# Kernel tuning notes

Hardware: AMD Instinct MI355X
Metric: run time of the kernel (lower is better)

The kernel has to match this reference:

```python
import jax, jax.numpy as jnp
import numpy as np

B, S, D, H = 2, 2048, 1024, 16
DH = D // H  # per-head dim = 64


def setup_inputs() -> dict:
    key = jax.random.key(0)
    k0, k1, k2, k3, k4, k5 = jax.random.split(key, 6)
    x = jax.random.normal(k0, (B, S, D), dtype=jnp.float32)
    # mask: True where token is valid, False where padded ([B, S, 1] bool)
    mask = jax.random.randint(k1, (B, S, 1), 0, 2).astype(bool)
    scale = 0.02
    # Per-head projection weights stacked over heads: [H, D, DH]
    Wq = jax.random.normal(k2, (H, D, DH), dtype=jnp.float32) * scale
    Wk = jax.random.normal(k3, (H, D, DH), dtype=jnp.float32) * scale
    Wv = jax.random.normal(k4, (H, D, DH), dtype=jnp.float32) * scale
    # Output projection, torch Linear convention [out, in]: y = out @ Wo.T
    Wo = jax.random.normal(k5, (D, D), dtype=jnp.float32) * scale
    return {"x": x, "mask": mask, "Wq": Wq, "Wk": Wk, "Wv": Wv, "Wo": Wo}


def reference(x, mask, Wq, Wk, Wv, Wo):
    # Batched per-head projections (equivalent to the per-head Linear loop)
    q = jnp.einsum('bsd,hde->bhse', x, Wq)  # [B,H,S,DH]
    k = jnp.einsum('bsd,hde->bhse', x, Wk)
    v = jnp.einsum('bsd,hde->bhse', x, Wv)
    scale = 1.0 / np.sqrt(DH).astype(np.float32)
    scores = jnp.einsum('bhqe,bhke->bhqk', q, k) * scale  # [B,H,S,S]
    key_mask = mask[:, None, None, :, 0]   # [B,1,1,S]
    qry_mask = mask[:, None, :, :]          # [B,1,S,1]
    # masked keys get -1e10 added (same as original: +(~key_mask)*-1e10)
    scores = scores + (~key_mask) * jnp.float32(-1e10)
    attn = jax.nn.softmax(scores, axis=-1)
    attn = attn * qry_mask                  # zero rows for padded queries
    ctx = jnp.einsum('bhqk,bhke->bhqe', attn, v)  # [B,H,S,DH]
    # concat heads along last dim (head h -> contiguous slice, matches torch.cat)
    out = ctx.transpose(0, 2, 1, 3).reshape(B, S, D)
    return out @ Wo.T
```

## Files before the change

### kernel.cpp

```cpp
#include <hip/hip_runtime.h>
#include <hip/hip_bf16.h>

typedef __attribute__((ext_vector_type(8))) short sh8;
typedef __attribute__((ext_vector_type(4))) float f32x4;

#define LDC 136
#define QSCALE 0.18033688f
#define KMBF16 0xF14Au

#define EXP2F(x) __builtin_amdgcn_exp2f(x)

__device__ __forceinline__ void glds16(const unsigned short* g, unsigned short* l){
  __builtin_amdgcn_global_load_lds(
      (const __attribute__((address_space(1))) unsigned int*)g,
      (__attribute__((address_space(3))) unsigned int*)l, 16, 0, 0);
}

__device__ __forceinline__ unsigned short f2bf(float f){
  union { float f; unsigned u; } c; c.f = f;
  unsigned u = c.u;
  u += 0x7fffu + ((u >> 16) & 1u);
  return (unsigned short)(u >> 16);
}

__device__ __forceinline__ unsigned long long pack4bf(float a, float b, float c, float d){
  __hip_bfloat162 lo = __float22bfloat162_rn(make_float2(a, b));
  __hip_bfloat162 hi = __float22bfloat162_rn(make_float2(c, d));
  union { unsigned u[2]; unsigned long long ull; } pk;
  pk.u[0] = *(unsigned*)&lo; pk.u[1] = *(unsigned*)&hi;
  return pk.ull;
}

__global__ __launch_bounds__(256) void cvt_bf16_2(const float* __restrict__ s0,
                                                  unsigned short* __restrict__ d0, int n0,
                                                  const float* __restrict__ s1,
                                                  unsigned short* __restrict__ d1, int n1){
  int i = blockIdx.x*256 + threadIdx.x;
  const float* s; unsigned short* d;
  if (i < n0){ s = s0; d = d0; }
  else if (i < n0 + n1){ s = s1; d = d1; i -= n0; }
  else return;
  float4 v = ((const float4*)s)[i];
  ushort4 o;
  o.x = f2bf(v.x); o.y = f2bf(v.y); o.z = f2bf(v.z); o.w = f2bf(v.w);
  ((ushort4*)d)[i] = o;
}

__global__ __launch_bounds__(256) void transpose_w(const float* __restrict__ Wq,
                                                   const float* __restrict__ Wk,
                                                   const float* __restrict__ Wv,
                                                   unsigned short* __restrict__ wt){
  __shared__ float tile[64][65];
  int idx = blockIdx.x;
  int jm = idx >> 8;
  int rest = idx & 255;
  int h = rest >> 4, dt = rest & 15;
  const float* src = (jm==0 ? Wq : (jm==1 ? Wk : Wv)) + (size_t)h*65536;
  int t = threadIdx.x;
  {
    int r = t >> 2, c0 = (t & 3)*16;
    for (int i=0;i<4;++i){
      float4 v = *(const float4*)&src[(size_t)(dt*64 + r)*64 + c0 + i*4];
      tile[r][c0+i*4+0]=v.x; tile[r][c0+i*4+1]=v.y; tile[r][c0+i*4+2]=v.z; tile[r][c0+i*4+3]=v.w;
    }
  }
  __syncthreads();
  {
    int e = t >> 2, r0 = (t & 3)*16;
    int j = jm*1024 + h*64 + e;
    __align__(16) unsigned short buf[16];
    for (int i=0;i<16;++i) buf[i] = f2bf(tile[r0+i][e]);
    *(uint4*)&wt[(size_t)j*1024 + dt*64 + r0    ] = *(uint4*)&buf[0];
    *(uint4*)&wt[(size_t)j*1024 + dt*64 + r0 + 8] = *(uint4*)&buf[8];
  }
}

template<int BM>
__global__ __launch_bounds__(256) void gemm_bt(const unsigned short* __restrict__ A,
                                               const unsigned short* __restrict__ Bt,
                                               unsigned short* __restrict__ Cq,
                                               unsigned short* __restrict__ Ck,
                                               unsigned short* __restrict__ Cv,
                                               float* __restrict__ Cf,
                                               int M, int N, int K, int mode){
  constexpr int MI = BM/32;
  constexpr int ABUF = BM*64;
  constexpr int DBUFN = 2*ABUF + 2*8192;
  constexpr int SMEMN = (DBUFN > 17408) ? DBUFN : 17408;
  __shared__ __align__(16) unsigned short smem[SMEMN];
  const int t = threadIdx.x;
  const int w = t >> 6, lane = t & 63, l15 = lane & 15, quad = lane >> 4;

  int lin = blockIdx.y * gridDim.x + blockIdx.x;
  int gn = gridDim.x;
  int per = 8 * gn;
  int gid = lin / per, rem = lin % per;
  int j = rem / gn, nc = rem % gn;
  const int m0 = (gid*8 + j) * BM;
  const int n0 = nc * 128;

  const int wm = (w >> 1)*(BM/2), wn = (w & 1)*64;
  const int lr8 = lane >> 3;
  const int gc8 = (lane & 7) ^ lr8;
  const int h7 = l15 & 7;
  f32x4 acc[MI][4] = {};

  auto stage = [&](int k0, int bb){
    unsigned short* as = smem + bb*ABUF;
    unsigned short* bs = smem + 2*ABUF + bb*8192;
    for (int p = 0; p < BM/32; ++p){
      int rbase = p*32 + w*8;
      glds16(&A [(size_t)(m0 + rbase + lr8)*K + k0 + gc8*8], &as[rbase*64]);
    }
    for (int p = 0; p < 4; ++p){
      int rbase = p*32 + w*8;
      glds16(&Bt[(size_t)(n0 + rbase + lr8)*K + k0 + gc8*8], &bs[rbase*64]);
    }
  };

  const int NS = K >> 6;
  stage(0, 0);
  for (int ks = 0; ks < NS; ++ks){
    const int bb = ks & 1;
    __syncthreads();
    if (ks + 1 < NS) stage((ks+1)*64, bb ^ 1);
    const unsigned short* as = smem + bb*ABUF;
    const unsigned short* bs = smem + 2*ABUF + bb*8192;
    for (int kk = 0; kk < 2; ++kk){
      const int cs = (((kk<<2) + quad) ^ h7) * 8;
      sh8 aF[MI], bF[4];
      for (int i = 0; i < MI; ++i)
        aF[i] = *(const sh8*)&as[(wm + i*16 + l15)*64 + cs];
      for (int i = 0; i < 4; ++i)
        bF[i] = *(const sh8*)&bs[(wn + i*16 + l15)*64 + cs];
      for (int mi = 0; mi < MI; ++mi)
        for (int ni = 0; ni < 4; ++ni)
          acc[mi][ni] = __builtin_amdgcn_mfma_f32_16x16x32_bf16(aF[mi], bF[ni], acc[mi][ni], 0, 0, 0);
    }
  }

  if (mode == 2){
    for (int mi = 0; mi < MI; ++mi){
      int rowb = m0 + wm + mi*16 + quad*4;
      for (int ni = 0; ni < 4; ++ni){
        int col = n0 + wn + ni*16 + l15;
        for (int r = 0; r < 4; ++r)
          Cf[(size_t)(rowb + r)*N + col] = acc[mi][ni][r];
      }
    }
    return;
  }

  if constexpr (BM == 128){
    __syncthreads();
    unsigned short* Ct = smem;
    const bool isv = (n0 >= 2048);
    const float cscale = (n0 < 1024) ? QSCALE : 1.0f;
    for (int mi = 0; mi < 4; ++mi){
      for (int ni = 0; ni < 4; ++ni){
        for (int r = 0; r < 4; ++r){
          int lr = wm + mi*16 + quad*4 + r;
          int lc = wn + ni*16 + l15;
          unsigned short bv = f2bf(acc[mi][ni][r] * cscale);
          if (isv) Ct[lc*LDC + lr] = bv;
          else     Ct[lr*LDC + lc] = bv;
        }
      }
    }
    __syncthreads();

    const int b = m0 >> 11, sbase = m0 & 2047;
    const int hbase = (n0 & 1023) >> 6;
    if (!isv){
      unsigned short* dst = (n0 < 1024) ? Cq : Ck;
      for (int i = 0; i < 8; ++i){
        int s  = i*16 + (t >> 4);
        int hh = (t >> 3) & 1;
        int c  = t & 7;
        uint4 val = *(const uint4*)&Ct[s*LDC + hh*64 + c*8];
        int h = hbase + hh;
        *(uint4*)&dst[((size_t)(b*16 + h)*2048 + sbase + s)*64 + c*8] = val;
      }
    } else {
      for (int i = 0; i < 8; ++i){
        int ecol = i*16 + (t >> 4);
        int s0   = (t & 15)*8;
        uint4 val = *(const uint4*)&Ct[ecol*LDC + s0];
        int hh = ecol >> 6, e = ecol & 63;
        int h = hbase + hh;
        *(uint4*)&Cv[((size_t)(b*16 + h)*64 + e)*2048 + sbase + s0] = val;
      }
    }
  }
}

__global__ __launch_bounds__(512) void flash_attn(const unsigned short* __restrict__ q,
                                                  const unsigned short* __restrict__ k,
                                                  const unsigned short* __restrict__ vt,
                                                  const int* __restrict__ mask,
                                                  unsigned short* __restrict__ ctx){
  __shared__ __align__(16) unsigned short Ks[2][4096];
  __shared__ __align__(16) unsigned short Vs[2][4096];
  __shared__ __align__(16) unsigned short Ps[8][1024];
  __shared__ __align__(16) unsigned short kmb[2048];

  const int idx = blockIdx.x;
  const int xcd = idx & 7, sub = idx >> 3;
  const int bh = xcd*4 + (sub & 3);
  const int qt = sub >> 2;
  const int b = bh >> 4, h = bh & 15;
  const int t = threadIdx.x;
  const int w = t >> 6, lane = t & 63, l15 = lane & 15, quad = lane >> 4;
  const size_t base = (size_t)bh * 2048 * 64;

  const unsigned short* qp0 = q + base + (size_t)(qt*128 + w*16 + l15)*64;
  sh8 qf[2];
  qf[0] = *(const sh8*)(qp0 +      quad*8);
  qf[1] = *(const sh8*)(qp0 + 32 + quad*8);

  {
    int4 m0 = ((const int4*)(mask + b*2048))[t];
    __align__(8) unsigned short tmp[4];
    tmp[0] = m0.x ? 0 : KMBF16; tmp[1] = m0.y ? 0 : KMBF16;
    tmp[2] = m0.z ? 0 : KMBF16; tmp[3] = m0.w ? 0 : KMBF16;
    *(unsigned long long*)&kmb[t*4] = *(unsigned long long*)tmp;
  }

  const int lr8 = lane >> 3;
  const int gc8 = (lane & 7) ^ lr8;
  const int h7 = l15 & 7;
  const int cs0 = ((quad    ) ^ h7) * 8;
  const int cs1 = ((quad + 4) ^ h7) * 8;
  const int pw_off = (quad & 1)*4;
  const int pr0 = ((0*4 + quad) ^ h7) * 8;
  const int pr1 = ((1*4 + quad) ^ h7) * 8;

  auto stageKV = [&](int kt, int bb){
    int r0 = w*8;
    glds16(&k [base + (size_t)(kt*64 + r0 + lr8)*64 + gc8*8], &Ks[bb][r0*64]);
    glds16(&vt[base + (size_t)(r0 + lr8)*2048 + kt*64 + gc8*8], &Vs[bb][r0*64]);
  };

  float la[4] = {};
  f32x4 O[4] = {};

  stageKV(0, 0);
  for (int kt = 0; kt < 32; ++kt){
    const int bb = kt & 1;
    __syncthreads();
    if (kt + 1 < 32) stageKV(kt + 1, bb ^ 1);

    for (int mt = 0; mt < 4; ++mt){
      sh8 a0 = *(const sh8*)&Ks[bb][(mt*16 + l15)*64 + cs0];
      sh8 a1 = *(const sh8*)&Ks[bb][(mt*16 + l15)*64 + cs1];
      unsigned long long kq = *(const unsigned long long*)&kmb[kt*64 + mt*16 + quad*4];
      unsigned d0 = (unsigned)kq, d1 = (unsigned)(kq >> 32);
      f32x4 a;
      a[0] = __uint_as_float(d0 << 16);
      a[1] = __uint_as_float(d0 & 0xFFFF0000u);
      a[2] = __uint_as_float(d1 << 16);
      a[3] = __uint_as_float(d1 & 0xFFFF0000u);
      const int pwc = (((mt*2 + (quad>>1)) ^ h7) * 8) + pw_off;
      a = __builtin_amdgcn_mfma_f32_16x16x32_bf16(a0, qf[0], a, 0, 0, 0);
      a = __builtin_amdgcn_mfma_f32_16x16x32_bf16(a1, qf[1], a, 0, 0, 0);
      float e0 = EXP2F(a[0]); la[0] += e0;
      float e1 = EXP2F(a[1]); la[1] += e1;
      float e2 = EXP2F(a[2]); la[2] += e2;
      float e3 = EXP2F(a[3]); la[3] += e3;
      *(unsigned long long*)&Ps[w][l15*64 + pwc] = pack4bf(e0, e1, e2, e3);
    }

    sh8 pf0 = *(const sh8*)&Ps[w][l15*64 + pr0];
    sh8 pf1 = *(const sh8*)&Ps[w][l15*64 + pr1];
    for (int et = 0; et < 4; ++et){
      sh8 vf0 = *(const sh8*)&Vs[bb][(et*16 + l15)*64 + cs0];
      O[et] = __builtin_amdgcn_mfma_f32_16x16x32_bf16(vf0, pf0, O[et], 0, 0, 0);
    }
    for (int et = 0; et < 4; ++et){
      sh8 vf1 = *(const sh8*)&Vs[bb][(et*16 + l15)*64 + cs1];
      O[et] = __builtin_amdgcn_mfma_f32_16x16x32_bf16(vf1, pf1, O[et], 0, 0, 0);
    }
  }

  {
    float l_i = (la[0] + la[1]) + (la[2] + la[3]);
    l_i += __shfl_xor(l_i, 16);
    l_i += __shfl_xor(l_i, 32);
    int srow = qt*128 + w*16 + l15;
    bool qm = (kmb[srow] == 0);
    float inv = (qm && l_i > 0.f) ? 1.f/l_i : 0.f;
    unsigned short* crow = ctx + (((size_t)b*2048 + srow)*16 + h)*64;
    for (int et = 0; et < 4; ++et)
      *(unsigned long long*)&crow[et*16 + quad*4] =
        pack4bf(O[et][0]*inv, O[et][1]*inv, O[et][2]*inv, O[et][3]*inv);
  }
}

extern "C" void kernel_launch(void* const* d_in, const int* in_sizes, int n_in,
                              void* d_out, int out_size, void* d_ws, size_t ws_size,
                              hipStream_t stream){
  const float* x  = (const float*)d_in[0];
  const int* mask = (const int*)  d_in[1];
  const float* Wq = (const float*)d_in[2];
  const float* Wk = (const float*)d_in[3];
  const float* Wv = (const float*)d_in[4];
  const float* Wo = (const float*)d_in[5];
  float* out = (float*)d_out;

  char* ws = (char*)d_ws;
  unsigned short* x_bf  = (unsigned short*)(ws);
  unsigned short* wt    = (unsigned short*)(ws + 8388608);
  unsigned short* wo_bf = (unsigned short*)(ws + 14680064);
  unsigned short* qb    = (unsigned short*)(ws + 16777216);
  unsigned short* kb    = (unsigned short*)(ws + 25165824);
  unsigned short* vtb   = (unsigned short*)(ws + 33554432);
  unsigned short* ctx   = (unsigned short*)(ws + 41943040);

  cvt_bf16_2<<<5120, 256, 0, stream>>>(x, x_bf, 1048576, Wo, wo_bf, 262144);
  transpose_w<<<768, 256, 0, stream>>>(Wq, Wk, Wv, wt);
  gemm_bt<128><<<dim3(24, 32), 256, 0, stream>>>(x_bf, wt, qb, kb, vtb, nullptr, 4096, 3072, 1024, 0);
  flash_attn<<<512, 512, 0, stream>>>(qb, kb, vtb, mask, ctx);
  gemm_bt<64><<<dim3(8, 64), 256, 0, stream>>>(ctx, wo_bf, nullptr, nullptr, nullptr, out, 4096, 1024, 1024, 2);
}
```

Baseline: 184.4 us.

## Split attention over key halves and pass P through registers via permlane swaps

Attention now splits the key sequence in two, launching twice as many blocks. Each block writes unnormalized partial outputs and row sums, and a new reduce kernel adds the halves, normalizes and applies the query mask. Separately, the P tile no longer goes through a shared-memory round trip: the bf16 probabilities are rearranged with v_permlane32/16_swap to form the MFMA B operand directly, which frees LDS and removes per-tile LDS traffic. The trade-off is an extra launch and an extra read/write of two bf16 partial buffers, plus bf16 rounding of the partials before summation.

```diff
diff --git a/kernel.cpp b/kernel.cpp
--- a/kernel.cpp
+++ b/kernel.cpp
@@ -29,6 +29,13 @@
   union { unsigned u[2]; unsigned long long ull; } pk;
   pk.u[0] = *(unsigned*)&lo; pk.u[1] = *(unsigned*)&hi;
   return pk.ull;
+}
+
+__device__ __forceinline__ void pl32swap(unsigned &a, unsigned &b){
+  asm volatile("v_permlane32_swap_b32 %0, %1" : "+v"(a), "+v"(b));
+}
+__device__ __forceinline__ void pl16swap(unsigned &a, unsigned &b){
+  asm volatile("v_permlane16_swap_b32 %0, %1" : "+v"(a), "+v"(b));
 }
 
 __global__ __launch_bounds__(256) void cvt_bf16_2(const float* __restrict__ s0,
@@ -198,32 +205,37 @@
                                                   const unsigned short* __restrict__ k,
                                                   const unsigned short* __restrict__ vt,
                                                   const int* __restrict__ mask,
-                                                  unsigned short* __restrict__ ctx){
+                                                  unsigned short* __restrict__ O0,
+                                                  unsigned short* __restrict__ O1,
+                                                  float* __restrict__ l0,
+                                                  float* __restrict__ l1){
   __shared__ __align__(16) unsigned short Ks[2][4096];
   __shared__ __align__(16) unsigned short Vs[2][4096];
-  __shared__ __align__(16) unsigned short Ps[8][1024];
-  __shared__ __align__(16) unsigned short kmb[2048];
+  __shared__ __align__(16) unsigned short kmb[1024];
 
   const int idx = blockIdx.x;
   const int xcd = idx & 7, sub = idx >> 3;
   const int bh = xcd*4 + (sub & 3);
-  const int qt = sub >> 2;
+  const int qrest = sub >> 2;
+  const int qt = qrest & 15;
+  const int half = qrest >> 4;
+  const int hk0 = half << 10;
   const int b = bh >> 4, h = bh & 15;
   const int t = threadIdx.x;
   const int w = t >> 6, lane = t & 63, l15 = lane & 15, quad = lane >> 4;
   const size_t base = (size_t)bh * 2048 * 64;
 
+  unsigned short* Op = half ? O1 : O0;
+  float*          lp = half ? l1 : l0;
+
   const unsigned short* qp0 = q + base + (size_t)(qt*128 + w*16 + l15)*64;
   sh8 qf[2];
   qf[0] = *(const sh8*)(qp0 +      quad*8);
   qf[1] = *(const sh8*)(qp0 + 32 + quad*8);
 
   {
-    int4 m0 = ((const int4*)(mask + b*2048))[t];
-    __align__(8) unsigned short tmp[4];
-    tmp[0] = m0.x ? 0 : KMBF16; tmp[1] = m0.y ? 0 : KMBF16;
-    tmp[2] = m0.z ? 0 : KMBF16; tmp[3] = m0.w ? 0 : KMBF16;
-    *(unsigned long long*)&kmb[t*4] = *(unsigned long long*)tmp;
+    int2 mv = ((const int2*)(mask + b*2048 + hk0))[t];
+    ((unsigned*)kmb)[t] = (mv.x ? 0u : (unsigned)KMBF16) | ((mv.y ? 0u : (unsigned)KMBF16) << 16);
   }
 
   const int lr8 = lane >> 3;
@@ -231,25 +243,23 @@
   const int h7 = l15 & 7;
   const int cs0 = ((quad    ) ^ h7) * 8;
   const int cs1 = ((quad + 4) ^ h7) * 8;
-  const int pw_off = (quad & 1)*4;
-  const int pr0 = ((0*4 + quad) ^ h7) * 8;
-  const int pr1 = ((1*4 + quad) ^ h7) * 8;
 
   auto stageKV = [&](int kt, int bb){
     int r0 = w*8;
-    glds16(&k [base + (size_t)(kt*64 + r0 + lr8)*64 + gc8*8], &Ks[bb][r0*64]);
-    glds16(&vt[base + (size_t)(r0 + lr8)*2048 + kt*64 + gc8*8], &Vs[bb][r0*64]);
+    glds16(&k [base + (size_t)(hk0 + kt*64 + r0 + lr8)*64 + gc8*8], &Ks[bb][r0*64]);
+    glds16(&vt[base + (size_t)(r0 + lr8)*2048 + hk0 + kt*64 + gc8*8], &Vs[bb][r0*64]);
   };
 
   float la[4] = {};
   f32x4 O[4] = {};
 
   stageKV(0, 0);
-  for (int kt = 0; kt < 32; ++kt){
+  for (int kt = 0; kt < 16; ++kt){
     const int bb = kt & 1;
     __syncthreads();
-    if (kt + 1 < 32) stageKV(kt + 1, bb ^ 1);
-
+    if (kt + 1 < 16) stageKV(kt + 1, bb ^ 1);
+
+    unsigned ed[4][2];
     for (int mt = 0; mt < 4; ++mt){
       sh8 a0 = *(const sh8*)&Ks[bb][(mt*16 + l15)*64 + cs0];
       sh8 a1 = *(const sh8*)&Ks[bb][(mt*16 + l15)*64 + cs1];
@@ -260,22 +270,38 @@
       a[1] = __uint_as_float(d0 & 0xFFFF0000u);
       a[2] = __uint_as_float(d1 << 16);
       a[3] = __uint_as_float(d1 & 0xFFFF0000u);
-      const int pwc = (((mt*2 + (quad>>1)) ^ h7) * 8) + pw_off;
       a = __builtin_amdgcn_mfma_f32_16x16x32_bf16(a0, qf[0], a, 0, 0, 0);
       a = __builtin_amdgcn_mfma_f32_16x16x32_bf16(a1, qf[1], a, 0, 0, 0);
       float e0 = EXP2F(a[0]); la[0] += e0;
       float e1 = EXP2F(a[1]); la[1] += e1;
       float e2 = EXP2F(a[2]); la[2] += e2;
       float e3 = EXP2F(a[3]); la[3] += e3;
-      *(unsigned long long*)&Ps[w][l15*64 + pwc] = pack4bf(e0, e1, e2, e3);
-    }
-
-    sh8 pf0 = *(const sh8*)&Ps[w][l15*64 + pr0];
-    sh8 pf1 = *(const sh8*)&Ps[w][l15*64 + pr1];
+      __hip_bfloat162 lo = __float22bfloat162_rn(make_float2(e0, e1));
+      __hip_bfloat162 hi = __float22bfloat162_rn(make_float2(e2, e3));
+      ed[mt][0] = *(unsigned*)&lo;
+      ed[mt][1] = *(unsigned*)&hi;
+    }
+
+    union { unsigned u[8]; sh8 s[2]; } pf;
+    #pragma unroll
+    for (int g = 0; g < 2; ++g){
+      #pragma unroll
+      for (int d = 0; d < 2; ++d){
+        unsigned A = ed[2*g][d], Bv = ed[2*g+1][d];
+        pl32swap(A, Bv);
+        pl16swap(A, Bv);
+        pf.u[g*4 + d]     = A;
+        pf.u[g*4 + d + 2] = Bv;
+      }
+    }
+    sh8 pf0 = pf.s[0], pf1 = pf.s[1];
+
+    #pragma unroll
     for (int et = 0; et < 4; ++et){
       sh8 vf0 = *(const sh8*)&Vs[bb][(et*16 + l15)*64 + cs0];
       O[et] = __builtin_amdgcn_mfma_f32_16x16x32_bf16(vf0, pf0, O[et], 0, 0, 0);
     }
+    #pragma unroll
     for (int et = 0; et < 4; ++et){
       sh8 vf1 = *(const sh8*)&Vs[bb][(et*16 + l15)*64 + cs1];
       O[et] = __builtin_amdgcn_mfma_f32_16x16x32_bf16(vf1, pf1, O[et], 0, 0, 0);
@@ -287,13 +313,37 @@
     l_i += __shfl_xor(l_i, 16);
     l_i += __shfl_xor(l_i, 32);
     int srow = qt*128 + w*16 + l15;
-    bool qm = (kmb[srow] == 0);
-    float inv = (qm && l_i > 0.f) ? 1.f/l_i : 0.f;
-    unsigned short* crow = ctx + (((size_t)b*2048 + srow)*16 + h)*64;
+    if (quad == 0) lp[(size_t)bh*2048 + srow] = l_i;
+    unsigned short* crow = Op + (((size_t)b*2048 + srow)*16 + h)*64;
     for (int et = 0; et < 4; ++et)
       *(unsigned long long*)&crow[et*16 + quad*4] =
-        pack4bf(O[et][0]*inv, O[et][1]*inv, O[et][2]*inv, O[et][3]*inv);
-  }
+        pack4bf(O[et][0], O[et][1], O[et][2], O[et][3]);
+  }
+}
+
+__global__ __launch_bounds__(256) void attn_reduce(const unsigned short* __restrict__ O0,
+                                                   const unsigned short* __restrict__ O1,
+                                                   const float* __restrict__ l0,
+                                                   const float* __restrict__ l1,
+                                                   const int* __restrict__ mask,
+                                                   unsigned short* __restrict__ ctx){
+  int gid = blockIdx.x*256 + threadIdx.x;
+  int h = (gid >> 3) & 15, s = (gid >> 7) & 2047, b = gid >> 18;
+  size_t off = (size_t)gid * 8;
+  union { uint4 v; unsigned u[4]; } ua, uc, ur;
+  ua.v = *(const uint4*)&O0[off];
+  uc.v = *(const uint4*)&O1[off];
+  int li = (b*16 + h)*2048 + s;
+  float l = l0[li] + l1[li];
+  float inv = (mask[b*2048 + s] && l > 0.f) ? 1.f/l : 0.f;
+  #pragma unroll
+  for (int i = 0; i < 4; ++i){
+    float e0 = (__uint_as_float(ua.u[i] << 16) + __uint_as_float(uc.u[i] << 16)) * inv;
+    float e1 = (__uint_as_float(ua.u[i] & 0xFFFF0000u) + __uint_as_float(uc.u[i] & 0xFFFF0000u)) * inv;
+    __hip_bfloat162 p = __float22bfloat162_rn(make_float2(e0, e1));
+    ur.u[i] = *(unsigned*)&p;
+  }
+  *(uint4*)&ctx[off] = ur.v;
 }
 
 extern "C" void kernel_launch(void* const* d_in, const int* in_sizes, int n_in,
@@ -314,11 +364,16 @@
   unsigned short* qb    = (unsigned short*)(ws + 16777216);
   unsigned short* kb    = (unsigned short*)(ws + 25165824);
   unsigned short* vtb   = (unsigned short*)(ws + 33554432);
-  unsigned short* ctx   = (unsigned short*)(ws + 41943040);
+  unsigned short* Of0   = (unsigned short*)(ws);
+  float*          l0    = (float*)(ws + 8388608);
+  float*          l1    = (float*)(ws + 8388608 + 262144);
+  unsigned short* Of1   = (unsigned short*)(ws + 41943040);
+  unsigned short* ctx   = (unsigned short*)(ws + 16777216);
 
   cvt_bf16_2<<<5120, 256, 0, stream>>>(x, x_bf, 1048576, Wo, wo_bf, 262144);
   transpose_w<<<768, 256, 0, stream>>>(Wq, Wk, Wv, wt);
   gemm_bt<128><<<dim3(24, 32), 256, 0, stream>>>(x_bf, wt, qb, kb, vtb, nullptr, 4096, 3072, 1024, 0);
-  flash_attn<<<512, 512, 0, stream>>>(qb, kb, vtb, mask, ctx);
+  flash_attn<<<1024, 512, 0, stream>>>(qb, kb, vtb, mask, Of0, Of1, l0, l1);
+  attn_reduce<<<2048, 256, 0, stream>>>(Of0, Of1, l0, l1, mask, ctx);
   gemm_bt<64><<<dim3(8, 64), 256, 0, stream>>>(ctx, wo_bf, nullptr, nullptr, nullptr, out, 4096, 1024, 1024, 2);
 }
```

After: 192.7 us. 1.05x slower.

## Compact valid keys and values so attention skips masked key tiles

Applied to the files above, without the earlier changes.

A new scan kernel computes a prefix-sum position for every valid token and zero-pads the tail of the packed K and V^T buffers. The QKV GEMM epilogue scatters K and V rows into these compacted positions. Flash attention counts the valid keys and loops only over ceil(nv/64) key tiles instead of all 32, which cuts its work roughly in proportion to the padding rate. In exchange the V^T store becomes a scalar per-element scatter instead of vector stores, and the workspace reuse for pidx overlaps the ctx buffer (ctx is written after pidx is last read by the projection, so this works as ordered).

```diff
diff --git a/kernel.cpp b/kernel.cpp
--- a/kernel.cpp
+++ b/kernel.cpp
@@ -75,6 +75,31 @@
   }
 }
 
+__global__ __launch_bounds__(256) void mask_scan(const int* __restrict__ mask,
+                                                 int* __restrict__ pidx,
+                                                 unsigned short* __restrict__ kb,
+                                                 unsigned short* __restrict__ vtb){
+  int b = blockIdx.x;
+  int t = threadIdx.x, w = t >> 6, lane = t & 63;
+  int base = 0;
+  for (int c = 0; c < 32; ++c){
+    int m = mask[b*2048 + c*64 + lane];
+    unsigned long long bal = __ballot(m != 0);
+    int pos = base + __popcll(bal & ((1ULL << lane) - 1ULL));
+    if (w == 0) pidx[b*2048 + c*64 + lane] = m ? pos : -1;
+    base += (int)__popcll(bal);
+  }
+  int nv = base;
+  int pend = (nv + 63) & ~63;
+  for (int h = w*4; h < w*4 + 4; ++h){
+    for (int row = nv; row < pend; ++row)
+      kb[((size_t)(b*16 + h)*2048 + row)*64 + lane] = 0;
+    for (int e = 0; e < 64; ++e)
+      for (int col = nv + lane; col < pend; col += 64)
+        vtb[((size_t)(b*16 + h)*64 + e)*2048 + col] = 0;
+  }
+}
+
 template<int BM>
 __global__ __launch_bounds__(256) void gemm_bt(const unsigned short* __restrict__ A,
                                                const unsigned short* __restrict__ Bt,
@@ -82,11 +107,12 @@
                                                unsigned short* __restrict__ Ck,
                                                unsigned short* __restrict__ Cv,
                                                float* __restrict__ Cf,
+                                               const int* __restrict__ pidx,
                                                int M, int N, int K, int mode){
   constexpr int MI = BM/32;
   constexpr int ABUF = BM*64;
   constexpr int DBUFN = 2*ABUF + 2*8192;
-  constexpr int SMEMN = (DBUFN > 17408) ? DBUFN : 17408;
+  constexpr int SMEMN = (DBUFN > 17664) ? DBUFN : 17664;
   __shared__ __align__(16) unsigned short smem[SMEMN];
   const int t = threadIdx.x;
   const int w = t >> 6, lane = t & 63, l15 = lane & 15, quad = lane >> 4;
@@ -154,8 +180,10 @@
   if constexpr (BM == 128){
     __syncthreads();
     unsigned short* Ct = smem;
+    int* pS = (int*)(smem + 17408);
     const bool isv = (n0 >= 2048);
     const float cscale = (n0 < 1024) ? QSCALE : 1.0f;
+    const int b = m0 >> 11, sbase = m0 & 2047;
     for (int mi = 0; mi < 4; ++mi){
       for (int ni = 0; ni < 4; ++ni){
         for (int r = 0; r < 4; ++r){
@@ -167,28 +195,36 @@
         }
       }
     }
+    if (t < 128) pS[t] = pidx[b*2048 + sbase + t];
     __syncthreads();
 
-    const int b = m0 >> 11, sbase = m0 & 2047;
     const int hbase = (n0 & 1023) >> 6;
     if (!isv){
-      unsigned short* dst = (n0 < 1024) ? Cq : Ck;
+      const bool isq = (n0 < 1024);
+      unsigned short* dst = isq ? Cq : Ck;
       for (int i = 0; i < 8; ++i){
         int s  = i*16 + (t >> 4);
         int hh = (t >> 3) & 1;
         int c  = t & 7;
         uint4 val = *(const uint4*)&Ct[s*LDC + hh*64 + c*8];
         int h = hbase + hh;
-        *(uint4*)&dst[((size_t)(b*16 + h)*2048 + sbase + s)*64 + c*8] = val;
+        int row;
+        if (isq) row = sbase + s;
+        else { int p = pS[s]; if (p < 0) continue; row = p; }
+        *(uint4*)&dst[((size_t)(b*16 + h)*2048 + row)*64 + c*8] = val;
       }
     } else {
       for (int i = 0; i < 8; ++i){
         int ecol = i*16 + (t >> 4);
         int s0   = (t & 15)*8;
-        uint4 val = *(const uint4*)&Ct[ecol*LDC + s0];
         int hh = ecol >> 6, e = ecol & 63;
         int h = hbase + hh;
-        *(uint4*)&Cv[((size_t)(b*16 + h)*64 + e)*2048 + sbase + s0] = val;
+        unsigned short* dr = &Cv[((size_t)(b*16 + h)*64 + e)*2048];
+        #pragma unroll
+        for (int jj = 0; jj < 8; ++jj){
+          int p = pS[s0 + jj];
+          if (p >= 0) dr[p] = Ct[ecol*LDC + s0 + jj];
+        }
       }
     }
   }
@@ -203,6 +239,7 @@
   __shared__ __align__(16) unsigned short Vs[2][4096];
   __shared__ __align__(16) unsigned short Ps[8][1024];
   __shared__ __align__(16) unsigned short kmb[2048];
+  __shared__ int s_nv;
 
   const int idx = blockIdx.x;
   const int xcd = idx & 7, sub = idx >> 3;
@@ -218,11 +255,23 @@
   qf[0] = *(const sh8*)(qp0 +      quad*8);
   qf[1] = *(const sh8*)(qp0 + 32 + quad*8);
 
-  {
-    int4 m0 = ((const int4*)(mask + b*2048))[t];
+  if (t == 0) s_nv = 0;
+  int4 mv = ((const int4*)(mask + b*2048))[t];
+  __syncthreads();
+  {
+    int c = (mv.x != 0) + (mv.y != 0) + (mv.z != 0) + (mv.w != 0);
+    c += __shfl_down(c, 32); c += __shfl_down(c, 16); c += __shfl_down(c, 8);
+    c += __shfl_down(c, 4);  c += __shfl_down(c, 2);  c += __shfl_down(c, 1);
+    if (lane == 0) atomicAdd(&s_nv, c);
+  }
+  __syncthreads();
+  const int nv = s_nv;
+  const int ntiles = (nv + 63) >> 6;
+
+  {
     __align__(8) unsigned short tmp[4];
-    tmp[0] = m0.x ? 0 : KMBF16; tmp[1] = m0.y ? 0 : KMBF16;
-    tmp[2] = m0.z ? 0 : KMBF16; tmp[3] = m0.w ? 0 : KMBF16;
+    #pragma unroll
+    for (int i = 0; i < 4; ++i) tmp[i] = (t*4 + i < nv) ? 0 : (unsigned short)KMBF16;
     *(unsigned long long*)&kmb[t*4] = *(unsigned long long*)tmp;
   }
 
@@ -244,11 +293,11 @@
   float la[4] = {};
   f32x4 O[4] = {};
 
-  stageKV(0, 0);
-  for (int kt = 0; kt < 32; ++kt){
+  if (ntiles > 0) stageKV(0, 0);
+  for (int kt = 0; kt < ntiles; ++kt){
     const int bb = kt & 1;
     __syncthreads();
-    if (kt + 1 < 32) stageKV(kt + 1, bb ^ 1);
+    if (kt + 1 < ntiles) stageKV(kt + 1, bb ^ 1);
 
     for (int mt = 0; mt < 4; ++mt){
       sh8 a0 = *(const sh8*)&Ks[bb][(mt*16 + l15)*64 + cs0];
@@ -287,7 +336,7 @@
     l_i += __shfl_xor(l_i, 16);
     l_i += __shfl_xor(l_i, 32);
     int srow = qt*128 + w*16 + l15;
-    bool qm = (kmb[srow] == 0);
+    bool qm = (mask[b*2048 + srow] != 0);
     float inv = (qm && l_i > 0.f) ? 1.f/l_i : 0.f;
     unsigned short* crow = ctx + (((size_t)b*2048 + srow)*16 + h)*64;
     for (int et = 0; et < 4; ++et)
@@ -315,10 +364,12 @@
   unsigned short* kb    = (unsigned short*)(ws + 25165824);
   unsigned short* vtb   = (unsigned short*)(ws + 33554432);
   unsigned short* ctx   = (unsigned short*)(ws + 41943040);
-
+  int*            pidx  = (int*)(ws + 41943040);
+
+  mask_scan<<<2, 256, 0, stream>>>(mask, pidx, kb, vtb);
   cvt_bf16_2<<<5120, 256, 0, stream>>>(x, x_bf, 1048576, Wo, wo_bf, 262144);
   transpose_w<<<768, 256, 0, stream>>>(Wq, Wk, Wv, wt);
-  gemm_bt<128><<<dim3(24, 32), 256, 0, stream>>>(x_bf, wt, qb, kb, vtb, nullptr, 4096, 3072, 1024, 0);
+  gemm_bt<128><<<dim3(24, 32), 256, 0, stream>>>(x_bf, wt, qb, kb, vtb, nullptr, pidx, 4096, 3072, 1024, 0);
   flash_attn<<<512, 512, 0, stream>>>(qb, kb, vtb, mask, ctx);
-  gemm_bt<64><<<dim3(8, 64), 256, 0, stream>>>(ctx, wo_bf, nullptr, nullptr, nullptr, out, 4096, 1024, 1024, 2);
-}
+  gemm_bt<64><<<dim3(8, 64), 256, 0, stream>>>(ctx, wo_bf, nullptr, nullptr, nullptr, out, pidx, 4096, 1024, 1024, 2);
+}
```

Result: slower. 205.8 us (+11.6%).
